# Kernel optimization log

Hardware: AMD Instinct MI355X
Metric: run time of the kernel (lower is better)

The kernel has to match this reference:

```python
import jax, jax.numpy as jnp
import numpy as np

N_USER, N_ITEM, D = 100000, 50000, 64
H, S, B, L, SUPP, E, HID = 4, 500, 1024, 50, 10000, 1500000, 64

def setup_inputs() -> dict:
    key = jax.random.key(0)
    ks = jax.random.split(key, 24)
    f = lambda k, shp: (jax.random.normal(k, shp, jnp.float32) * 0.1)
    inp = {
        'x': jax.random.randint(ks[0], (B, 2), 0, 50000),
        'history': jax.random.randint(ks[1], (B, L), 0, N_ITEM),
        'history_len': jax.random.randint(ks[2], (B,), 1, L + 1),
        'sample_index': jax.random.randint(ks[3], (H, B, S), 0, SUPP),
        'supp_users': jax.random.randint(ks[4], (SUPP,), 0, N_USER),
        'edge_index': jax.random.randint(ks[5], (2, E), 0, 50000),
        'user_embedding': f(ks[6], (N_USER, D)),
        'item_embedding': f(ks[7], (N_ITEM, D)),
        'wq': f(ks[8], (H, D, D)),
        'wk': f(ks[9], (H, D, D)),
        'wv': f(ks[10], (H, D, D)),
        'w_out_w': f(ks[11], (H * D, D)),
        'gcn_user_w': f(ks[12], (D, D)), 'gcn_user_b': jnp.full((D,), 0.1, jnp.float32),
        'gcn_item_w': f(ks[13], (D, D)), 'gcn_item_b': jnp.full((D,), 0.1, jnp.float32),
        'l1_w': f(ks[14], (4 * D, 2 * HID)), 'l1_b': jnp.full((2 * HID,), 0.1, jnp.float32),
        'l2_w': f(ks[15], (2 * HID, HID)), 'l2_b': jnp.full((HID,), 0.1, jnp.float32),
        'l3_w': f(ks[16], (HID, 1)), 'l3_b': jnp.full((1,), 0.1, jnp.float32),
        'user_bias': jnp.zeros((N_USER, 1), jnp.float32),
        'item_bias': jnp.zeros((N_ITEM, 1), jnp.float32),
    }
    return inp


def _forward(x, history, history_len, sample_index, supp_users, edge_index,
             user_embedding, item_embedding, wq, wk, wv, w_out_w,
             gcn_user_w, gcn_user_b, gcn_item_w, gcn_item_b,
             l1_w, l1_b, l2_w, l2_b, l3_w, l3_b, user_bias, item_bias):
    user_id = x[:, 0]
    item_id = x[:, 1]
    # user init embedding: mean of history item embeddings (original sums unmasked, divides by len)
    user_init_emb = jnp.sum(item_embedding[history], axis=1) / history_len[:, None].astype(jnp.float32)  # [B,D]

    # multi-head RelationGAT over randomly sampled support users
    samp_emb = user_embedding[supp_users[sample_index]]            # [H,B,S,D]
    q = jnp.einsum('bd,hde->hbe', user_init_emb, wq)               # [H,B,D]
    k = jnp.einsum('hbsd,hde->hbse', samp_emb, wk)                 # [H,B,S,D]
    attn = jax.nn.softmax(jnp.einsum('hbe,hbse->hbs', q, k), axis=-1)
    ctx = jnp.einsum('hbs,hbse->hbe', attn, k)                     # [H,B,D]
    gat = jnp.einsum('hbe,hef->hbf', ctx, wv)                      # [H,B,D]
    gat = jnp.transpose(gat, (1, 0, 2)).reshape(gat.shape[1], -1)  # [B,H*D]
    user_emb = gat @ w_out_w                                       # [B,D]

    item_emb = item_embedding[item_id]

    # sparse GCN aggregation via segment_sum (eval mode: no edge dropout)
    eu, ei = edge_index[0], edge_index[1]
    ones_e = jnp.ones((eu.shape[0],), jnp.float32)
    agg_item = jax.ops.segment_sum(item_embedding[ei], eu, num_segments=N_USER)[user_id]
    agg_user = jax.ops.segment_sum(user_embedding[eu], ei, num_segments=N_ITEM)[item_id]
    deg_u = jax.ops.segment_sum(ones_e, eu, num_segments=N_USER)[user_id][:, None] + 1.0
    deg_i = jax.ops.segment_sum(ones_e, ei, num_segments=N_ITEM)[item_id][:, None] + 1.0
    gcn_item_h = agg_item / deg_u
    gcn_user_h = agg_user / deg_i
    gcn_user_out = jax.nn.relu(gcn_user_h @ gcn_user_w + gcn_user_b)
    gcn_item_out = jax.nn.relu(gcn_item_h @ gcn_item_w + gcn_item_b)

    feats = jnp.concatenate([user_emb * item_emb,
                             user_emb * gcn_item_out,
                             gcn_user_out * item_emb,
                             gcn_user_out * gcn_item_out], axis=-1)  # [B,4D]
    h1 = jnp.tanh(feats @ l1_w + l1_b)
    h2 = jnp.tanh(h1 @ l2_w + l2_b)
    score = (h2 @ l3_w + l3_b).reshape(-1)
    return score + user_bias[user_id].reshape(-1) + item_bias[item_id].reshape(-1)


def reference(x, history, history_len, sample_index, supp_users, edge_index,
              user_embedding, item_embedding, wq, wk, wv, w_out_w,
              gcn_user_w, gcn_user_b, gcn_item_w, gcn_item_b,
              l1_w, l1_b, l2_w, l2_b, l3_w, l3_b, user_bias, item_bias):
    return _forward(x, history, history_len, sample_index, supp_users, edge_index,
                    user_embedding, item_embedding, wq, wk, wv, w_out_w,
                    gcn_user_w, gcn_user_b, gcn_item_w, gcn_item_b,
                    l1_w, l1_b, l2_w, l2_b, l3_w, l3_b, user_bias, item_bias)
```

## Files before the change

### kernel.cpp

```cpp
#include <hip/hip_runtime.h>
#include <hip/hip_bf16.h>
#include <math.h>

#define N_USER 100000
#define N_ITEM 50000
#define D 64
#define H 4
#define S 500
#define B 1024
#define L 50
#define SUPP 10000
#define E_EDGES 1500000
#define HID 64
#define N_ID 50000
#define CAP 256

#define SUPP_BLKS 625
#define UINIT_BLKS 256
#define PREP1_BLKS 32
#define PREP2_BLKS 64
#define REP_BLKS 4
#define B_UINIT (SUPP_BLKS)
#define B_PREP1 (B_UINIT + UINIT_BLKS)
#define B_PREP2 (B_PREP1 + PREP1_BLKS)
#define B_REP   (B_PREP2 + PREP2_BLKS)
#define SETUP_BLKS (B_REP + REP_BLKS)

__global__ void k_setup(const int* x, const int* history, const int* history_len,
                        const int* supp_users, const float* user_embedding,
                        const float* item_embedding, const float* wq, const float* wk,
                        const float* wv, const float* w_out_w,
                        float* supp_emb, float* uinit, float* Mmat, float* Pmat,
                        int* user_rep, int* item_rep, int* uctr, int* ictr) {
  __shared__ float smem[64 * 65];
  int blk = blockIdx.x, tid = threadIdx.x;
  if (blk < B_UINIT) {
    int i = blk * 256 + tid;
    if (i < SUPP * 16) {
      int r = i >> 4, c = i & 15;
      *(float4*)&supp_emb[r * 64 + c * 4] =
          *(const float4*)&user_embedding[(long)supp_users[r] * 64 + c * 4];
    }
  } else if (blk < B_PREP1) {
    int b = (blk - B_UINIT) * 4 + (tid >> 6);
    int lane = tid & 63, g = lane >> 4, sub = lane & 15;
    float4 acc = {0.f, 0.f, 0.f, 0.f};
    for (int l = g; l < L; l += 4) {
      int idx = history[b * L + l];
      float4 r = *(const float4*)&item_embedding[(long)idx * 64 + sub * 4];
      acc.x += r.x; acc.y += r.y; acc.z += r.z; acc.w += r.w;
    }
    acc.x += __shfl_xor(acc.x, 16); acc.y += __shfl_xor(acc.y, 16);
    acc.z += __shfl_xor(acc.z, 16); acc.w += __shfl_xor(acc.w, 16);
    acc.x += __shfl_xor(acc.x, 32); acc.y += __shfl_xor(acc.y, 32);
    acc.z += __shfl_xor(acc.z, 32); acc.w += __shfl_xor(acc.w, 32);
    if (lane < 16) {
      float inv = 1.f / (float)history_len[b];
      float4 o = {acc.x * inv, acc.y * inv, acc.z * inv, acc.w * inv};
      *(float4*)&uinit[b * 64 + lane * 4] = o;
    }
  } else if (blk < B_PREP2) {
    int local = blk - B_PREP1;
    int h = local >> 3, bx = local & 7;
    for (int i = tid; i < 64 * 64; i += 256) {
      int row = i >> 6, e = i & 63;
      smem[row * 65 + e] = wk[((long)h * 64 + row) * 64 + e];
    }
    __syncthreads();
    for (int k = 0; k < 2; k++) {
      int oidx = bx * 512 + k * 256 + tid;
      int dp = oidx >> 6, d = oidx & 63;
      float acc = 0.f;
      const float* wqrow = wq + ((long)h * 64 + dp) * 64;
#pragma unroll
      for (int e = 0; e < 64; e++) acc += wqrow[e] * smem[d * 65 + e];
      Mmat[((long)h * 64 + dp) * 64 + d] = acc;
    }
  } else if (blk < B_REP) {
    int local = blk - B_PREP2;
    int p = tid >> 6, lane = tid & 63;
    int gp = local * 4 + p;
    int h = gp >> 6, row = gp & 63;
    float* T = smem + p * 64;
    float tf = 0.f;
#pragma unroll
    for (int e = 0; e < 64; e++)
      tf += wk[((long)h * 64 + row) * 64 + e] * wv[((long)h * 64 + e) * 64 + lane];
    T[lane] = tf;
    __syncthreads();
    float acc = 0.f;
#pragma unroll
    for (int f = 0; f < 64; f++)
      acc += T[f] * w_out_w[((long)h * 64 + f) * 64 + lane];
    Pmat[((long)h * 64 + row) * 64 + lane] = acc;
  } else {
    int gi = (blk - B_REP) * 256 + tid;
    if (gi < B) {
      user_rep[x[2 * gi]] = gi;
      item_rep[x[2 * gi + 1]] = gi;
      uctr[gi] = 0;
      ictr[gi] = 0;
    }
  }
}

template <int CTRL>
__device__ __forceinline__ float dpp_add(float v) {
  int t = __builtin_amdgcn_update_dpp(0, __float_as_int(v), CTRL, 0xF, 0xF, true);
  return v + __int_as_float(t);
}
#define DPP_XOR1  0xB1
#define DPP_XOR2  0x4E
#define DPP_ROR4  0x124
#define DPP_ROR8  0x128

__global__ void k_attn(const float* uinit, const float* supp_emb, const int* sample_index,
                       const float* Mmat, const float* Pmat, float* uem4) {
  int b = blockIdx.x, h = blockIdx.y;
  int tid = threadIdx.x, w = tid >> 6, lane = tid & 63;
  int g = lane >> 4, sub = lane & 15;
  __shared__ float sm_u[64], sm_kq[64], sm_p[256], sm_part[256], sm_den[4];
  __shared__ int sm_sidx[512];

  const int* sidx = sample_index + ((long)h * B + b) * S;
  for (int i = tid; i < 512; i += 256) sm_sidx[i] = (i < S) ? sidx[i] : 0;
  if (tid < 64) sm_u[tid] = uinit[b * 64 + tid];
  __syncthreads();

  const float* Mh = Mmat + h * 64 * 64;
  {
    float p = 0.f;
#pragma unroll
    for (int j = 0; j < 16; j++) p += sm_u[w * 16 + j] * Mh[(w * 16 + j) * 64 + lane];
    sm_p[tid] = p;
  }
  __syncthreads();
  if (tid < 64) sm_kq[tid] = sm_p[tid] + sm_p[64 + tid] + sm_p[128 + tid] + sm_p[192 + tid];
  __syncthreads();

  float4 kq4 = *(float4*)&sm_kq[sub * 4];
  float4 acc = {0.f, 0.f, 0.f, 0.f};
  float den = 0.f;
#pragma unroll 4
  for (int it = 0; it < 32; it++) {
    int s = it * 16 + w * 4 + g;
    int idx = sm_sidx[s];
    float4 r = *(const float4*)&supp_emb[idx * 64 + sub * 4];
    float dot = r.x * kq4.x + r.y * kq4.y + r.z * kq4.z + r.w * kq4.w;
    dot = dpp_add<DPP_XOR1>(dot);
    dot = dpp_add<DPP_XOR2>(dot);
    dot = dpp_add<DPP_ROR4>(dot);
    dot = dpp_add<DPP_ROR8>(dot);
    float e = (s < S) ? __expf(dot) : 0.f;
    den += e;
    acc.x += e * r.x; acc.y += e * r.y; acc.z += e * r.z; acc.w += e * r.w;
  }
  den += __shfl_xor(den, 16); den += __shfl_xor(den, 32);
  acc.x += __shfl_xor(acc.x, 16); acc.y += __shfl_xor(acc.y, 16);
  acc.z += __shfl_xor(acc.z, 16); acc.w += __shfl_xor(acc.w, 16);
  acc.x += __shfl_xor(acc.x, 32); acc.y += __shfl_xor(acc.y, 32);
  acc.z += __shfl_xor(acc.z, 32); acc.w += __shfl_xor(acc.w, 32);
  if (lane < 16) {
    *(float4*)&sm_part[w * 64 + lane * 4] = acc;
    if (lane == 0) sm_den[w] = den;
  }
  __syncthreads();
  if (tid < 64) {
    float ws_ = sm_part[tid] + sm_part[64 + tid] + sm_part[128 + tid] + sm_part[192 + tid];
    float dn = sm_den[0] + sm_den[1] + sm_den[2] + sm_den[3];
    sm_u[tid] = ws_ / dn;
  }
  __syncthreads();
  const float* Ph = Pmat + h * 64 * 64;
  {
    float p = 0.f;
#pragma unroll
    for (int j = 0; j < 16; j++) p += sm_u[w * 16 + j] * Ph[(w * 16 + j) * 64 + lane];
    sm_p[tid] = p;
  }
  __syncthreads();
  if (tid < 64)
    uem4[((long)h * B + b) * 64 + tid] =
        sm_p[tid] + sm_p[64 + tid] + sm_p[128 + tid] + sm_p[192 + tid];
}

__device__ __forceinline__ void edge_probe(int u, int it, const int* x,
                                           const int* user_rep, const int* item_rep,
                                           int* uctr, int* ubin, int* ictr, int* ibin) {
  int ru = user_rep[u];
  if ((unsigned)ru < B && x[2 * ru] == u) {
    int pos = atomicAdd(&uctr[ru], 1);
    if (pos < CAP) ubin[ru * CAP + pos] = it;
  }
  int ri = item_rep[it];
  if ((unsigned)ri < B && x[2 * ri + 1] == it) {
    int pos = atomicAdd(&ictr[ri], 1);
    if (pos < CAP) ibin[ri * CAP + pos] = u;
  }
}

__global__ void k_edges(const int* eu, const int* ei, const int* x,
                        const int* user_rep, const int* item_rep,
                        int* uctr, int* ubin, int* ictr, int* ibin) {
  int i = blockIdx.x * blockDim.x + threadIdx.x;
  if (i >= E_EDGES / 4) return;
  int4 u4 = ((const int4*)eu)[i];
  int4 v4 = ((const int4*)ei)[i];
  edge_probe(u4.x, v4.x, x, user_rep, item_rep, uctr, ubin, ictr, ibin);
  edge_probe(u4.y, v4.y, x, user_rep, item_rep, uctr, ubin, ictr, ibin);
  edge_probe(u4.z, v4.z, x, user_rep, item_rep, uctr, ubin, ictr, ibin);
  edge_probe(u4.w, v4.w, x, user_rep, item_rep, uctr, ubin, ictr, ibin);
}

__global__ void k_gather(const int* uctr, const int* ubin, const int* ictr, const int* ibin,
                         const float* user_embedding, const float* item_embedding,
                         float* agg_item_c, float* agg_user_c, float* deg_u, float* deg_i) {
  int b = blockIdx.x, side = blockIdx.y, tid = threadIdx.x;
  const int* ctr = side == 0 ? uctr : ictr;
  const int* binb = (side == 0 ? ubin : ibin) + b * CAP;
  const float* emb = side == 0 ? item_embedding : user_embedding;
  int cnt = min(ctr[b], CAP);
  float s0 = 0.f, s1 = 0.f, s2 = 0.f, s3 = 0.f;
  int m = 0;
  for (; m + 3 < cnt; m += 4) {
    s0 += emb[(long)binb[m] * 64 + tid];
    s1 += emb[(long)binb[m + 1] * 64 + tid];
    s2 += emb[(long)binb[m + 2] * 64 + tid];
    s3 += emb[(long)binb[m + 3] * 64 + tid];
  }
  for (; m < cnt; m++) s0 += emb[(long)binb[m] * 64 + tid];
  float tot = (s0 + s1) + (s2 + s3);
  if (side == 0) {
    agg_item_c[b * 64 + tid] = tot;
    if (tid == 0) deg_u[b] = (float)cnt;
  } else {
    agg_user_c[b * 64 + tid] = tot;
    if (tid == 0) deg_i[b] = (float)cnt;
  }
}

__global__ void k_final(const int* x, const float* uem4, const float* item_embedding,
                        const int* user_rep, const int* item_rep,
                        const float* agg_item_c, const float* agg_user_c,
                        const float* deg_u, const float* deg_i,
                        const float* gcn_user_w, const float* gcn_user_b,
                        const float* gcn_item_w, const float* gcn_item_b,
                        const float* l1_w, const float* l1_b,
                        const float* l2_w, const float* l2_b,
                        const float* l3_w, const float* l3_b,
                        const float* user_bias, const float* item_bias, float* out) {
  int b = blockIdx.x, tid = threadIdx.x;
  __shared__ float ue[D], ie[D], guh[D], gih[D], guo[D], gio[D],
      feats[4 * D], h1[2 * HID], h2[HID];
  int uid = x[2 * b], iid = x[2 * b + 1];
  if (tid < D) {
    ue[tid] = uem4[(0L * B + b) * D + tid] + uem4[(1L * B + b) * D + tid] +
              uem4[(2L * B + b) * D + tid] + uem4[(3L * B + b) * D + tid];
    ie[tid] = item_embedding[(long)iid * D + tid];
    int ru = user_rep[uid], ri = item_rep[iid];
    gih[tid] = agg_item_c[ru * D + tid] / (deg_u[ru] + 1.f);
    guh[tid] = agg_user_c[ri * D + tid] / (deg_i[ri] + 1.f);
  }
  __syncthreads();
  if (tid < D) {
    float a = 0.f, c = 0.f;
    for (int d = 0; d < D; d++) {
      a += guh[d] * gcn_user_w[d * D + tid];
      c += gih[d] * gcn_item_w[d * D + tid];
    }
    guo[tid] = fmaxf(a + gcn_user_b[tid], 0.f);
    gio[tid] = fmaxf(c + gcn_item_b[tid], 0.f);
  }
  __syncthreads();
  if (tid < D) {
    feats[tid]         = ue[tid] * ie[tid];
    feats[D + tid]     = ue[tid] * gio[tid];
    feats[2 * D + tid] = guo[tid] * ie[tid];
    feats[3 * D + tid] = guo[tid] * gio[tid];
  }
  __syncthreads();
  {
    float a = 0.f;
    for (int i = 0; i < 4 * D; i++) a += feats[i] * l1_w[i * (2 * HID) + tid];
    h1[tid] = tanhf(a + l1_b[tid]);
  }
  __syncthreads();
  if (tid < HID) {
    float a = 0.f;
    for (int i = 0; i < 2 * HID; i++) a += h1[i] * l2_w[i * HID + tid];
    h2[tid] = tanhf(a + l2_b[tid]);
  }
  __syncthreads();
  if (tid < 64) {
    float v = h2[tid] * l3_w[tid];
#pragma unroll
    for (int off = 32; off > 0; off >>= 1) v += __shfl_xor(v, off);
    if (tid == 0)
      out[b] = v + l3_b[0] + user_bias[uid] + item_bias[iid];
  }
}

extern "C" void kernel_launch(void* const* d_in, const int* in_sizes, int n_in,
                              void* d_out, int out_size, void* d_ws, size_t ws_size,
                              hipStream_t stream) {
  const int* x             = (const int*)d_in[0];
  const int* history       = (const int*)d_in[1];
  const int* history_len   = (const int*)d_in[2];
  const int* sample_index  = (const int*)d_in[3];
  const int* supp_users    = (const int*)d_in[4];
  const int* edge_index    = (const int*)d_in[5];
  const float* user_embedding = (const float*)d_in[6];
  const float* item_embedding = (const float*)d_in[7];
  const float* wq       = (const float*)d_in[8];
  const float* wk       = (const float*)d_in[9];
  const float* wv       = (const float*)d_in[10];
  const float* w_out_w  = (const float*)d_in[11];
  const float* gcn_user_w = (const float*)d_in[12];
  const float* gcn_user_b = (const float*)d_in[13];
  const float* gcn_item_w = (const float*)d_in[14];
  const float* gcn_item_b = (const float*)d_in[15];
  const float* l1_w = (const float*)d_in[16];
  const float* l1_b = (const float*)d_in[17];
  const float* l2_w = (const float*)d_in[18];
  const float* l2_b = (const float*)d_in[19];
  const float* l3_w = (const float*)d_in[20];
  const float* l3_b = (const float*)d_in[21];
  const float* user_bias = (const float*)d_in[22];
  const float* item_bias = (const float*)d_in[23];
  float* out = (float*)d_out;

  float* fws        = (float*)d_ws;
  float* agg_item_c = fws;
  float* agg_user_c = agg_item_c + B * D;
  float* deg_u      = agg_user_c + B * D;
  float* deg_i      = deg_u + B;
  float* uinit      = deg_i + B;
  float* supp_emb   = uinit + B * D;
  float* uem4       = supp_emb + (long)SUPP * D;
  float* Mmat       = uem4 + (long)H * B * D;
  float* Pmat       = Mmat + H * D * D;
  int* user_rep     = (int*)(Pmat + H * D * D);
  int* item_rep     = user_rep + N_ID;
  int* uctr         = item_rep + N_ID;
  int* ictr         = uctr + B;
  int* ubin         = ictr + B;
  int* ibin         = ubin + B * CAP;

  const int* eu = edge_index;
  const int* ei = edge_index + E_EDGES;

  k_setup<<<SETUP_BLKS, 256, 0, stream>>>(x, history, history_len, supp_users,
                                          user_embedding, item_embedding, wq, wk, wv,
                                          w_out_w, supp_emb, uinit, Mmat, Pmat,
                                          user_rep, item_rep, uctr, ictr);
  k_edges<<<(E_EDGES / 4 + 255) / 256, 256, 0, stream>>>(eu, ei, x, user_rep, item_rep,
                                                         uctr, ubin, ictr, ibin);
  dim3 ag(B, H);
  k_attn<<<ag, 256, 0, stream>>>(uinit, supp_emb, sample_index, Mmat, Pmat, uem4);
  dim3 gg(B, 2);
  k_gather<<<gg, 64, 0, stream>>>(uctr, ubin, ictr, ibin, user_embedding, item_embedding,
                                  agg_item_c, agg_user_c, deg_u, deg_i);
  k_final<<<B, 128, 0, stream>>>(x, uem4, item_embedding, user_rep, item_rep,
                                 agg_item_c, agg_user_c, deg_u, deg_i,
                                 gcn_user_w, gcn_user_b, gcn_item_w, gcn_item_b,
                                 l1_w, l1_b, l2_w, l2_b, l3_w, l3_b,
                                 user_bias, item_bias, out);
}
```

Baseline: 86.65 us.

## Merge edge binning with attention, fold gather into final, store support embeddings as bf16

The edge-binning and attention kernels now share one launch as disjoint block ranges, so the two independent workloads can overlap and one launch is removed. The neighbor gather kernel is folded into the final kernel, with the two 64-thread halves each aggregating one side, which drops a launch and the intermediate aggregate buffers. Support-user embeddings are stored as bf16 to halve the gather traffic in the attention loop, at the cost of reduced precision in the attention scores and weighted sums.

```diff
diff --git a/kernel.cpp b/kernel.cpp
--- a/kernel.cpp
+++ b/kernel.cpp
@@ -26,11 +26,18 @@
 #define B_REP   (B_PREP2 + PREP2_BLKS)
 #define SETUP_BLKS (B_REP + REP_BLKS)
 
+__device__ __forceinline__ ushort f2bf(float f) {
+  unsigned u = __float_as_uint(f);
+  return (ushort)((u + 0x7FFF + ((u >> 16) & 1)) >> 16);
+}
+__device__ __forceinline__ float bf_lo(unsigned v) { return __uint_as_float(v << 16); }
+__device__ __forceinline__ float bf_hi(unsigned v) { return __uint_as_float(v & 0xFFFF0000u); }
+
 __global__ void k_setup(const int* x, const int* history, const int* history_len,
                         const int* supp_users, const float* user_embedding,
                         const float* item_embedding, const float* wq, const float* wk,
                         const float* wv, const float* w_out_w,
-                        float* supp_emb, float* uinit, float* Mmat, float* Pmat,
+                        ushort* supp_bf, float* uinit, float* Mmat, float* Pmat,
                         int* user_rep, int* item_rep, int* uctr, int* ictr) {
   __shared__ float smem[64 * 65];
   int blk = blockIdx.x, tid = threadIdx.x;
@@ -38,8 +45,9 @@
     int i = blk * 256 + tid;
     if (i < SUPP * 16) {
       int r = i >> 4, c = i & 15;
-      *(float4*)&supp_emb[r * 64 + c * 4] =
-          *(const float4*)&user_embedding[(long)supp_users[r] * 64 + c * 4];
+      float4 v = *(const float4*)&user_embedding[(long)supp_users[r] * 64 + c * 4];
+      ushort4 o = {f2bf(v.x), f2bf(v.y), f2bf(v.z), f2bf(v.w)};
+      *(ushort4*)&supp_bf[r * 64 + c * 4] = o;
     }
   } else if (blk < B_PREP1) {
     int b = (blk - B_UINIT) * 4 + (tid >> 6);
@@ -114,10 +122,44 @@
 #define DPP_ROR4  0x124
 #define DPP_ROR8  0x128
 
-__global__ void k_attn(const float* uinit, const float* supp_emb, const int* sample_index,
-                       const float* Mmat, const float* Pmat, float* uem4) {
-  int b = blockIdx.x, h = blockIdx.y;
-  int tid = threadIdx.x, w = tid >> 6, lane = tid & 63;
+#define MID_EDGE ((E_EDGES / 4 + 255) / 256)
+#define MID_BLKS (MID_EDGE + B * H)
+
+__device__ __forceinline__ void edge_probe(int u, int it, const int* x,
+                                           const int* user_rep, const int* item_rep,
+                                           int* uctr, int* ubin, int* ictr, int* ibin) {
+  int ru = user_rep[u];
+  if ((unsigned)ru < B && x[2 * ru] == u) {
+    int pos = atomicAdd(&uctr[ru], 1);
+    if (pos < CAP) ubin[ru * CAP + pos] = it;
+  }
+  int ri = item_rep[it];
+  if ((unsigned)ri < B && x[2 * ri + 1] == it) {
+    int pos = atomicAdd(&ictr[ri], 1);
+    if (pos < CAP) ibin[ri * CAP + pos] = u;
+  }
+}
+
+__global__ void k_mid(const int* eu, const int* ei, const int* x,
+                      const int* user_rep, const int* item_rep,
+                      int* uctr, int* ubin, int* ictr, int* ibin,
+                      const float* uinit, const ushort* supp_bf, const int* sample_index,
+                      const float* Mmat, const float* Pmat, float* uem4) {
+  int tid = threadIdx.x;
+  if (blockIdx.x < MID_EDGE) {
+    int i = blockIdx.x * 256 + tid;
+    if (i >= E_EDGES / 4) return;
+    int4 u4 = ((const int4*)eu)[i];
+    int4 v4 = ((const int4*)ei)[i];
+    edge_probe(u4.x, v4.x, x, user_rep, item_rep, uctr, ubin, ictr, ibin);
+    edge_probe(u4.y, v4.y, x, user_rep, item_rep, uctr, ubin, ictr, ibin);
+    edge_probe(u4.z, v4.z, x, user_rep, item_rep, uctr, ubin, ictr, ibin);
+    edge_probe(u4.w, v4.w, x, user_rep, item_rep, uctr, ubin, ictr, ibin);
+    return;
+  }
+  int id = blockIdx.x - MID_EDGE;
+  int h = id >> 10, b = id & 1023;
+  int w = tid >> 6, lane = tid & 63;
   int g = lane >> 4, sub = lane & 15;
   __shared__ float sm_u[64], sm_kq[64], sm_p[256], sm_part[256], sm_den[4];
   __shared__ int sm_sidx[512];
@@ -145,15 +187,16 @@
   for (int it = 0; it < 32; it++) {
     int s = it * 16 + w * 4 + g;
     int idx = sm_sidx[s];
-    float4 r = *(const float4*)&supp_emb[idx * 64 + sub * 4];
-    float dot = r.x * kq4.x + r.y * kq4.y + r.z * kq4.z + r.w * kq4.w;
+    uint2 rv = *(const uint2*)&supp_bf[idx * 64 + sub * 4];
+    float r0 = bf_lo(rv.x), r1 = bf_hi(rv.x), r2 = bf_lo(rv.y), r3 = bf_hi(rv.y);
+    float dot = r0 * kq4.x + r1 * kq4.y + r2 * kq4.z + r3 * kq4.w;
     dot = dpp_add<DPP_XOR1>(dot);
     dot = dpp_add<DPP_XOR2>(dot);
     dot = dpp_add<DPP_ROR4>(dot);
     dot = dpp_add<DPP_ROR8>(dot);
     float e = (s < S) ? __expf(dot) : 0.f;
     den += e;
-    acc.x += e * r.x; acc.y += e * r.y; acc.z += e * r.z; acc.w += e * r.w;
+    acc.x += e * r0; acc.y += e * r1; acc.z += e * r2; acc.w += e * r3;
   }
   den += __shfl_xor(den, 16); den += __shfl_xor(den, 32);
   acc.x += __shfl_xor(acc.x, 16); acc.y += __shfl_xor(acc.y, 16);
@@ -184,65 +227,10 @@
         sm_p[tid] + sm_p[64 + tid] + sm_p[128 + tid] + sm_p[192 + tid];
 }
 
-__device__ __forceinline__ void edge_probe(int u, int it, const int* x,
-                                           const int* user_rep, const int* item_rep,
-                                           int* uctr, int* ubin, int* ictr, int* ibin) {
-  int ru = user_rep[u];
-  if ((unsigned)ru < B && x[2 * ru] == u) {
-    int pos = atomicAdd(&uctr[ru], 1);
-    if (pos < CAP) ubin[ru * CAP + pos] = it;
-  }
-  int ri = item_rep[it];
-  if ((unsigned)ri < B && x[2 * ri + 1] == it) {
-    int pos = atomicAdd(&ictr[ri], 1);
-    if (pos < CAP) ibin[ri * CAP + pos] = u;
-  }
-}
-
-__global__ void k_edges(const int* eu, const int* ei, const int* x,
+__global__ void k_final(const int* x, const float* uem4,
+                        const float* user_embedding, const float* item_embedding,
                         const int* user_rep, const int* item_rep,
-                        int* uctr, int* ubin, int* ictr, int* ibin) {
-  int i = blockIdx.x * blockDim.x + threadIdx.x;
-  if (i >= E_EDGES / 4) return;
-  int4 u4 = ((const int4*)eu)[i];
-  int4 v4 = ((const int4*)ei)[i];
-  edge_probe(u4.x, v4.x, x, user_rep, item_rep, uctr, ubin, ictr, ibin);
-  edge_probe(u4.y, v4.y, x, user_rep, item_rep, uctr, ubin, ictr, ibin);
-  edge_probe(u4.z, v4.z, x, user_rep, item_rep, uctr, ubin, ictr, ibin);
-  edge_probe(u4.w, v4.w, x, user_rep, item_rep, uctr, ubin, ictr, ibin);
-}
-
-__global__ void k_gather(const int* uctr, const int* ubin, const int* ictr, const int* ibin,
-                         const float* user_embedding, const float* item_embedding,
-                         float* agg_item_c, float* agg_user_c, float* deg_u, float* deg_i) {
-  int b = blockIdx.x, side = blockIdx.y, tid = threadIdx.x;
-  const int* ctr = side == 0 ? uctr : ictr;
-  const int* binb = (side == 0 ? ubin : ibin) + b * CAP;
-  const float* emb = side == 0 ? item_embedding : user_embedding;
-  int cnt = min(ctr[b], CAP);
-  float s0 = 0.f, s1 = 0.f, s2 = 0.f, s3 = 0.f;
-  int m = 0;
-  for (; m + 3 < cnt; m += 4) {
-    s0 += emb[(long)binb[m] * 64 + tid];
-    s1 += emb[(long)binb[m + 1] * 64 + tid];
-    s2 += emb[(long)binb[m + 2] * 64 + tid];
-    s3 += emb[(long)binb[m + 3] * 64 + tid];
-  }
-  for (; m < cnt; m++) s0 += emb[(long)binb[m] * 64 + tid];
-  float tot = (s0 + s1) + (s2 + s3);
-  if (side == 0) {
-    agg_item_c[b * 64 + tid] = tot;
-    if (tid == 0) deg_u[b] = (float)cnt;
-  } else {
-    agg_user_c[b * 64 + tid] = tot;
-    if (tid == 0) deg_i[b] = (float)cnt;
-  }
-}
-
-__global__ void k_final(const int* x, const float* uem4, const float* item_embedding,
-                        const int* user_rep, const int* item_rep,
-                        const float* agg_item_c, const float* agg_user_c,
-                        const float* deg_u, const float* deg_i,
+                        const int* uctr, const int* ubin, const int* ictr, const int* ibin,
                         const float* gcn_user_w, const float* gcn_user_b,
                         const float* gcn_item_w, const float* gcn_item_b,
                         const float* l1_w, const float* l1_b,
@@ -250,23 +238,46 @@
                         const float* l3_w, const float* l3_b,
                         const float* user_bias, const float* item_bias, float* out) {
   int b = blockIdx.x, tid = threadIdx.x;
-  __shared__ float ue[D], ie[D], guh[D], gih[D], guo[D], gio[D],
+  int side = tid >> 6, lane = tid & 63;
+  __shared__ float ue[D], ie[D], agg[2][D], degs[2], guo[D], gio[D],
       feats[4 * D], h1[2 * HID], h2[HID];
   int uid = x[2 * b], iid = x[2 * b + 1];
+
+  {
+    int rep = side == 0 ? user_rep[uid] : item_rep[iid];
+    int cnt = min((side == 0 ? uctr : ictr)[rep], CAP);
+    const int* bin = ((side == 0 ? ubin : ibin)) + rep * CAP;
+    const float* emb = side == 0 ? item_embedding : user_embedding;
+    float s0 = 0.f, s1 = 0.f, s2 = 0.f, s3 = 0.f;
+    int m = 0;
+    for (; m + 3 < cnt; m += 4) {
+      s0 += emb[(long)bin[m] * 64 + lane];
+      s1 += emb[(long)bin[m + 1] * 64 + lane];
+      s2 += emb[(long)bin[m + 2] * 64 + lane];
+      s3 += emb[(long)bin[m + 3] * 64 + lane];
+    }
+    for (; m < cnt; m++) s0 += emb[(long)bin[m] * 64 + lane];
+    agg[side][lane] = (s0 + s1) + (s2 + s3);
+    if (lane == 0) degs[side] = (float)cnt;
+  }
   if (tid < D) {
     ue[tid] = uem4[(0L * B + b) * D + tid] + uem4[(1L * B + b) * D + tid] +
               uem4[(2L * B + b) * D + tid] + uem4[(3L * B + b) * D + tid];
     ie[tid] = item_embedding[(long)iid * D + tid];
-    int ru = user_rep[uid], ri = item_rep[iid];
-    gih[tid] = agg_item_c[ru * D + tid] / (deg_u[ru] + 1.f);
-    guh[tid] = agg_user_c[ri * D + tid] / (deg_i[ri] + 1.f);
+  }
+  __syncthreads();
+  if (tid < D) {
+    float gih = agg[0][tid] / (degs[0] + 1.f);
+    float guh = agg[1][tid] / (degs[1] + 1.f);
+    agg[0][tid] = gih;
+    agg[1][tid] = guh;
   }
   __syncthreads();
   if (tid < D) {
     float a = 0.f, c = 0.f;
     for (int d = 0; d < D; d++) {
-      a += guh[d] * gcn_user_w[d * D + tid];
-      c += gih[d] * gcn_item_w[d * D + tid];
+      a += agg[1][d] * gcn_user_w[d * D + tid];
+      c += agg[0][d] * gcn_item_w[d * D + tid];
     }
     guo[tid] = fmaxf(a + gcn_user_b[tid], 0.f);
     gio[tid] = fmaxf(c + gcn_item_b[tid], 0.f);
@@ -330,13 +341,9 @@
   float* out = (float*)d_out;
 
   float* fws        = (float*)d_ws;
-  float* agg_item_c = fws;
-  float* agg_user_c = agg_item_c + B * D;
-  float* deg_u      = agg_user_c + B * D;
-  float* deg_i      = deg_u + B;
-  float* uinit      = deg_i + B;
-  float* supp_emb   = uinit + B * D;
-  float* uem4       = supp_emb + (long)SUPP * D;
+  float* uinit      = fws;
+  ushort* supp_bf   = (ushort*)(uinit + B * D);
+  float* uem4       = uinit + B * D + SUPP * D / 2;
   float* Mmat       = uem4 + (long)H * B * D;
   float* Pmat       = Mmat + H * D * D;
   int* user_rep     = (int*)(Pmat + H * D * D);
@@ -351,17 +358,13 @@
 
   k_setup<<<SETUP_BLKS, 256, 0, stream>>>(x, history, history_len, supp_users,
                                           user_embedding, item_embedding, wq, wk, wv,
-                                          w_out_w, supp_emb, uinit, Mmat, Pmat,
+                                          w_out_w, supp_bf, uinit, Mmat, Pmat,
                                           user_rep, item_rep, uctr, ictr);
-  k_edges<<<(E_EDGES / 4 + 255) / 256, 256, 0, stream>>>(eu, ei, x, user_rep, item_rep,
-                                                         uctr, ubin, ictr, ibin);
-  dim3 ag(B, H);
-  k_attn<<<ag, 256, 0, stream>>>(uinit, supp_emb, sample_index, Mmat, Pmat, uem4);
-  dim3 gg(B, 2);
-  k_gather<<<gg, 64, 0, stream>>>(uctr, ubin, ictr, ibin, user_embedding, item_embedding,
-                                  agg_item_c, agg_user_c, deg_u, deg_i);
-  k_final<<<B, 128, 0, stream>>>(x, uem4, item_embedding, user_rep, item_rep,
-                                 agg_item_c, agg_user_c, deg_u, deg_i,
+  k_mid<<<MID_BLKS, 256, 0, stream>>>(eu, ei, x, user_rep, item_rep,
+                                      uctr, ubin, ictr, ibin,
+                                      uinit, supp_bf, sample_index, Mmat, Pmat, uem4);
+  k_final<<<B, 128, 0, stream>>>(x, uem4, user_embedding, item_embedding,
+                                 user_rep, item_rep, uctr, ubin, ictr, ibin,
                                  gcn_user_w, gcn_user_b, gcn_item_w, gcn_item_b,
                                  l1_w, l1_b, l2_w, l2_b, l3_w, l3_b,
                                  user_bias, item_bias, out);
```

Result: faster. 76.94 us (-11.2%).
